# Kernel tuning notes

Measured on AMD Instinct MI355X. Metric: run time of the kernel, lower is better.

Reference implementation:

```python
import jax, jax.numpy as jnp
import numpy as np
from jax import lax

WINDOW_SIZE = 11
SIGMA = 1.5
DATA_RANGE = 1.0


def _gaussian_window(channels):
    coords = jnp.arange(WINDOW_SIZE, dtype=jnp.float32) - WINDOW_SIZE // 2
    g = jnp.exp(-coords ** 2 / (2.0 * SIGMA ** 2))
    g = g / g.sum()
    w2d = jnp.outer(g, g)
    w2d = w2d / w2d.sum()
    # depthwise kernel: (C, 1, K, K) in OIHW with feature_group_count=C
    return jnp.broadcast_to(w2d, (channels, 1, WINDOW_SIZE, WINDOW_SIZE))


def _dwconv(x, window, channels):
    pad = WINDOW_SIZE // 2
    return lax.conv_general_dilated(
        x, window,
        window_strides=(1, 1),
        padding=[(pad, pad), (pad, pad)],
        dimension_numbers=('NCHW', 'OIHW', 'NCHW'),
        feature_group_count=channels,
    )


def setup_inputs() -> dict:
    key = jax.random.key(0)
    k1, k2 = jax.random.split(key)
    B, C, H, W = 16, 3, 512, 512
    x = jax.random.uniform(k1, (B, C, H, W), dtype=jnp.float32)
    y = jax.random.uniform(k2, (B, C, H, W), dtype=jnp.float32)
    return {"x": x, "y": y}


def reference(x, y):
    channels = x.shape[1]
    window = _gaussian_window(channels)
    mu_x = _dwconv(x, window, channels)
    mu_y = _dwconv(y, window, channels)
    mu_x2 = mu_x * mu_x
    mu_y2 = mu_y * mu_y
    mu_xy = mu_x * mu_y
    sigma_x2 = _dwconv(x * x, window, channels) - mu_x2
    sigma_y2 = _dwconv(y * y, window, channels) - mu_y2
    sigma_xy = _dwconv(x * y, window, channels) - mu_xy
    c1 = (0.01 * DATA_RANGE) ** 2
    c2 = (0.03 * DATA_RANGE) ** 2
    ssim_map = (2 * mu_xy + c1) * (2 * sigma_xy + c2) / (
        (mu_x2 + mu_y2 + c1) * (sigma_x2 + sigma_y2 + c2) + 1e-08)
    per_image = ssim_map.mean(axis=(1, 2, 3))
    return 1.0 - per_image.mean()
```

## Files before the change

kernel.cpp:

```cpp
#include <hip/hip_runtime.h>
#include <math.h>


#define IMG_W 512
#define IMG_H 512
#define PLANES 48
#define TX 64
#define TYS 64
#define RAD 5
#define NT 256
#define GDX (IMG_W / TX)
#define GDY (IMG_H / TYS)
#define NBLK (GDX * GDY * PLANES)
#define NCH 5
#define CSTR 24
#define PSTR (TX * CSTR)
#define NUMREC (IMG_W * IMG_H * 4)
#define CHSTEP (16 * IMG_W * 4)
#define INVW  0.26601181f
#define GC2   0.32059890f

typedef _Float16 h2 __attribute__((ext_vector_type(2)));
typedef _Float16 h4 __attribute__((ext_vector_type(4)));
typedef _Float16 h8 __attribute__((ext_vector_type(8)));
typedef float f32x4 __attribute__((ext_vector_type(4)));
typedef int i32x4 __attribute__((ext_vector_type(4)));

__device__ f32x4 buf_ld_x4(i32x4 srsrc, int voffset, int soffset, int aux)
    __asm("llvm.amdgcn.raw.buffer.load.v4f32");

__device__ __forceinline__ i32x4 make_srd(const float* p) {
    union { i32x4 v; struct { const float* p; unsigned rng; unsigned cfg; } s; } u;
    u.s.p = p; u.s.rng = NUMREC; u.s.cfg = 0x00020000u;
    return u.v;
}

__device__ __forceinline__ float exp2_fast(float a) {
#if __has_builtin(__builtin_amdgcn_exp2f)
    return __builtin_amdgcn_exp2f(a);
#else
    return exp2f(a);
#endif
}

__device__ __forceinline__ float wbandf(int idx) {
    const float fd = (float)(idx - 5);
    const float g = exp2_fast(-(fd * fd) * GC2) * INVW;
    return ((unsigned)idx <= 10u) ? g : 0.f;
}

__device__ __forceinline__ h2 pkrtz(float a, float b) {
    auto t = __builtin_amdgcn_cvt_pkrtz(a, b);
    h2 r;
    __builtin_memcpy(&r, &t, sizeof(r));
    return r;
}

__device__ __forceinline__ h4 pack4(f32x4 a) {
    const h2 lo = pkrtz(a[0], a[1]), hi = pkrtz(a[2], a[3]);
    h4 v;
    v[0] = lo.x; v[1] = lo.y; v[2] = hi.x; v[3] = hi.y;
    return v;
}

__device__ __forceinline__ void hconv_chunk(
    f32x4 xa, f32x4 xb, f32x4 ya, f32x4 yb, h8 whB,
    _Float16* wp)
{
    const f32x4 zz = {0.f, 0.f, 0.f, 0.f};
    const h2 xh0 = pkrtz(xa[0], xa[1]), xh1 = pkrtz(xa[2], xa[3]);
    const h2 xh2 = pkrtz(xb[0], xb[1]), xh3 = pkrtz(xb[2], xb[3]);
    const h2 yh0 = pkrtz(ya[0], ya[1]), yh1 = pkrtz(ya[2], ya[3]);
    const h2 yh2 = pkrtz(yb[0], yb[1]), yh3 = pkrtz(yb[2], yb[3]);
    const h2 s0 = xh0 + yh0, s1 = xh1 + yh1, s2 = xh2 + yh2, s3 = xh3 + yh3;
    const h2 d0 = xh0 - yh0, d1 = xh1 - yh1, d2 = xh2 - yh2, d3 = xh3 - yh3;
    h8 sA, dA;
    sA[0] = s0.x; sA[1] = s0.y; sA[2] = s1.x; sA[3] = s1.y;
    sA[4] = s2.x; sA[5] = s2.y; sA[6] = s3.x; sA[7] = s3.y;
    dA[0] = d0.x; dA[1] = d0.y; dA[2] = d1.x; dA[3] = d1.y;
    dA[4] = d2.x; dA[5] = d2.y; dA[6] = d3.x; dA[7] = d3.y;
    const h8 s2A = sA * sA;
    const h8 d2A = dA * dA;
    const f32x4 hS  = __builtin_amdgcn_mfma_f32_16x16x32_f16(sA,  whB, zz, 0, 0, 0);
    const f32x4 hD  = __builtin_amdgcn_mfma_f32_16x16x32_f16(dA,  whB, zz, 0, 0, 0);
    const f32x4 hS2 = __builtin_amdgcn_mfma_f32_16x16x32_f16(s2A, whB, zz, 0, 0, 0);
    const f32x4 hD2 = __builtin_amdgcn_mfma_f32_16x16x32_f16(d2A, whB, zz, 0, 0, 0);
    *(h4*)(wp + 0 * PSTR) = pack4(hS);
    *(h4*)(wp + 1 * PSTR) = pack4(hD);
    *(h4*)(wp + 2 * PSTR) = pack4(hS2);
    *(h4*)(wp + 3 * PSTR) = pack4(hD2);
}

__device__ __forceinline__ float mapsum(f32x4 aS, f32x4 aD, f32x4 aS2, f32x4 aD2,
                                        float cv)
{
    float local = 0.f;
    #pragma unroll
    for (int r = 0; r < 4; ++r) {
        const float mS = aS[r]  * cv, mD = aD[r]  * cv;
        const float eS = aS2[r] * cv, eD = aD2[r] * cv;
        const float ms2 = mS * mS, md2 = mD * mD;
        const float Pm = 0.5f * (ms2 - md2);
        const float Qm = 0.5f * (ms2 + md2);
        const float Pe = 0.5f * (eS - eD);
        const float Qe = 0.5f * (eS + eD);
        const float c1 = 1e-4f, c2 = 9e-4f;
        const float num = (Pm + c1) * (Pe - Pm + c2);
        const float den = (Qm + c1) * (Qe - Qm + c2) + 1e-8f;
        local += num * __builtin_amdgcn_rcpf(den);
    }
    return local;
}

#define MFMA16(A, B, C) __builtin_amdgcn_mfma_f32_16x16x32_f16((A), (B), (C), 0, 0, 0)

#define VSTART(ACC) do {                         \
    ACC[0] = MFMA16(wvA1, B0, zz);               \
    ACC[1] = MFMA16(wvA1, B1, zz);               \
    ACC[2] = MFMA16(wvA1, B2, zz);               \
    ACC[3] = MFMA16(wvA1, B3, zz);               \
} while (0)

#define VFINISH(ACC) do {                        \
    const f32x4 fS  = MFMA16(wvA2, B0, ACC[0]);  \
    const f32x4 fD  = MFMA16(wvA2, B1, ACC[1]);  \
    const f32x4 fS2 = MFMA16(wvA2, B2, ACC[2]);  \
    const f32x4 fD2 = MFMA16(wvA2, B3, ACC[3]);  \
    local += mapsum(fS, fD, fS2, fD2, cv);       \
} while (0)

__global__ __launch_bounds__(NT, 5) void ssim_tile_kernel(
    const float* __restrict__ x, const float* __restrict__ y,
    float* __restrict__ partials)
{
    __shared__ __align__(16) _Float16 Ht[4 * PSTR];
    __shared__ float wave_sums[NT / 64];

    const int tid = threadIdx.x;
    const int l = tid & 63, wid = tid >> 6;
    const int q = l >> 4, fc = l & 15;

    const int plane = blockIdx.z;
    const i32x4 srdx = make_srd(x + (size_t)plane * IMG_H * IMG_W);
    const i32x4 srdy = make_srd(y + (size_t)plane * IMG_H * IMG_W);
    const int C0 = blockIdx.x * TX;
    const int R0 = blockIdx.y * TYS;
    const int c0 = 16 * wid;
    const int col = c0 + fc;
    const int gcol = C0 + c0 - 8 + 8 * q;
    const int gr0 = R0 - RAD + fc;
    int voff = ((unsigned)gcol < (unsigned)IMG_W)
             ? ((gr0 << 11) + (gcol << 2)) : 0x60000000;

    f32x4 LXA[2], LXB[2], LYA[2], LYB[2];
    #pragma unroll
    for (int cpl = 0; cpl < 2; ++cpl) {
        LXA[cpl] = buf_ld_x4(srdx, voff, 0, 0);
        LXB[cpl] = buf_ld_x4(srdx, voff, 16, 0);
        LYA[cpl] = buf_ld_x4(srdy, voff, 0, 0);
        LYB[cpl] = buf_ld_x4(srdy, voff, 16, 0);
        voff += CHSTEP;
    }
    __builtin_amdgcn_sched_barrier(0);

    float s2w = 0.f;
    #pragma unroll
    for (int k = 0; k <= 10; ++k) s2w += (float)(_Float16)wbandf(k);
    const float cv = 1.f / (s2w * s2w);

    h8 whB, wvA1, wvA2;
    #pragma unroll
    for (int e = 0; e < 8; ++e) {
        const int k = 8 * q + e;
        whB[e]  = (_Float16)wbandf(k - fc - 3);
        wvA1[e] = (_Float16)((k < 16) ? wbandf(k - fc)      : 0.f);
        wvA2[e] = (_Float16)((k < 16) ? wbandf(k + 16 - fc) : 0.f);
    }

    _Float16* const hw = Ht + col * CSTR + 4 * q;
    const _Float16* const rbase = Ht + col * CSTR + 8 * (q & 1);

    f32x4 acc0[4], acc1[4];
    const f32x4 zz = {0.f, 0.f, 0.f, 0.f};
    float local = 0.f;

    #pragma unroll
    for (int c = 0; c < NCH; ++c) {
        if (c >= 1) {
            const h8 B0 = *(const h8*)(rbase + 0 * PSTR);
            const h8 B1 = *(const h8*)(rbase + 1 * PSTR);
            const h8 B2 = *(const h8*)(rbase + 2 * PSTR);
            const h8 B3 = *(const h8*)(rbase + 3 * PSTR);
            if (c & 1) {
                if (c >= 2) VFINISH(acc1);
                VSTART(acc0);
            } else {
                if (c >= 2) VFINISH(acc0);
                VSTART(acc1);
            }
        }
        hconv_chunk(LXA[c & 1], LXB[c & 1], LYA[c & 1], LYB[c & 1], whB, hw);
        if (c + 2 < NCH) {
            LXA[c & 1] = buf_ld_x4(srdx, voff, 0, 0);
            LXB[c & 1] = buf_ld_x4(srdx, voff, 16, 0);
            LYA[c & 1] = buf_ld_x4(srdy, voff, 0, 0);
            LYB[c & 1] = buf_ld_x4(srdy, voff, 16, 0);
            voff += CHSTEP;
        }
        __builtin_amdgcn_sched_barrier(0);
    }

    {
        const h8 B0 = *(const h8*)(rbase + 0 * PSTR);
        const h8 B1 = *(const h8*)(rbase + 1 * PSTR);
        const h8 B2 = *(const h8*)(rbase + 2 * PSTR);
        const h8 B3 = *(const h8*)(rbase + 3 * PSTR);
        VFINISH(acc1);
    }

    #pragma unroll
    for (int off = 32; off > 0; off >>= 1)
        local += __shfl_down(local, off, 64);
    if (l == 0) wave_sums[wid] = local;
    __syncthreads();
    if (tid == 0) {
        const float s = wave_sums[0] + wave_sums[1] + wave_sums[2] + wave_sums[3];
        const int bid = blockIdx.x + GDX * (blockIdx.y + GDY * blockIdx.z);
        partials[bid] = s;
    }
}

__global__ __launch_bounds__(NT) void ssim_finalize_kernel(
    const float* __restrict__ partials, float* __restrict__ out)
{
    const int tid = threadIdx.x;
    double s = 0.0;
    #pragma unroll 4
    for (int i = tid; i < NBLK; i += NT) s += (double)partials[i];
    #pragma unroll
    for (int off = 32; off > 0; off >>= 1)
        s += __shfl_down(s, off, 64);
    __shared__ double ws_[NT / 64];
    const int lane = tid & 63, wv = tid >> 6;
    if (lane == 0) ws_[wv] = s;
    __syncthreads();
    if (tid == 0) {
        const double t = ws_[0] + ws_[1] + ws_[2] + ws_[3];
        const double n = (double)PLANES * IMG_H * IMG_W;
        out[0] = (float)(1.0 - t / n);
    }
}

extern "C" void kernel_launch(void* const* d_in, const int* in_sizes, int n_in,
                              void* d_out, int out_size, void* d_ws, size_t ws_size,
                              hipStream_t stream)
{
    const float* x = (const float*)d_in[0];
    const float* y = (const float*)d_in[1];
    float* out = (float*)d_out;
    float* partials = (float*)d_ws;

    dim3 grid(GDX, GDY, PLANES);
    ssim_tile_kernel<<<grid, NT, 0, stream>>>(x, y, partials);
    ssim_finalize_kernel<<<1, NT, 0, stream>>>(partials, out);
}
```

Before: 135.3 us.

## Make each wave own an independent 16x128 strip with a single vertical MFMA

Each wave now processes an independent 16-column by 128-row strip with its own LDS region, and blocks shrink to two waves. Wave-level partial sums go straight to global memory, so no block barrier or shared reduction is needed. The vertical pass now uses one MFMA per quantity on a 32-row window, using a double-buffered LDS ring with a parity offset, in place of the split two-MFMA accumulate. Taller strips amortize halo rows and the new launch bounds allow more resident blocks. In exchange, strips are only 16 columns wide, so the horizontal halo is reloaded more often, and the finalize kernel has more partials to sum.

```diff
diff --git a/kernel.cpp b/kernel.cpp
--- a/kernel.cpp
+++ b/kernel.cpp
@@ -5,16 +5,16 @@
 #define IMG_W 512
 #define IMG_H 512
 #define PLANES 48
-#define TX 64
-#define TYS 64
+#define TYS 128
 #define RAD 5
-#define NT 256
-#define GDX (IMG_W / TX)
-#define GDY (IMG_H / TYS)
-#define NBLK (GDX * GDY * PLANES)
-#define NCH 5
-#define CSTR 24
-#define PSTR (TX * CSTR)
+#define NT 128
+#define NWAVES (PLANES * 32 * (IMG_H / TYS))
+#define NBLKS (NWAVES / 2)
+#define NCH 9
+#define NCV 8
+#define CSTR 40
+#define PSTR (16 * CSTR)
+#define WSTR (4 * PSTR)
 #define NUMREC (IMG_W * IMG_H * 4)
 #define CHSTEP (16 * IMG_W * 4)
 #define INVW  0.26601181f
@@ -114,43 +114,28 @@
 
 #define MFMA16(A, B, C) __builtin_amdgcn_mfma_f32_16x16x32_f16((A), (B), (C), 0, 0, 0)
 
-#define VSTART(ACC) do {                         \
-    ACC[0] = MFMA16(wvA1, B0, zz);               \
-    ACC[1] = MFMA16(wvA1, B1, zz);               \
-    ACC[2] = MFMA16(wvA1, B2, zz);               \
-    ACC[3] = MFMA16(wvA1, B3, zz);               \
-} while (0)
-
-#define VFINISH(ACC) do {                        \
-    const f32x4 fS  = MFMA16(wvA2, B0, ACC[0]);  \
-    const f32x4 fD  = MFMA16(wvA2, B1, ACC[1]);  \
-    const f32x4 fS2 = MFMA16(wvA2, B2, ACC[2]);  \
-    const f32x4 fD2 = MFMA16(wvA2, B3, ACC[3]);  \
-    local += mapsum(fS, fD, fS2, fD2, cv);       \
-} while (0)
-
-__global__ __launch_bounds__(NT, 5) void ssim_tile_kernel(
+__global__ __launch_bounds__(NT, 7) void ssim_tile_kernel(
     const float* __restrict__ x, const float* __restrict__ y,
     float* __restrict__ partials)
 {
-    __shared__ __align__(16) _Float16 Ht[4 * PSTR];
-    __shared__ float wave_sums[NT / 64];
+    __shared__ __align__(16) _Float16 Ht[2 * WSTR];
 
     const int tid = threadIdx.x;
     const int l = tid & 63, wid = tid >> 6;
     const int q = l >> 4, fc = l & 15;
-
-    const int plane = blockIdx.z;
+    const int ql = q & 1, qh = q >> 1;
+
+    const int gid = blockIdx.x * 2 + wid;
+    const int plane = gid >> 7;
+    const int rem = gid & 127;
+    const int R0 = (rem >> 5) * TYS;
+    const int C0 = (rem & 31) * 16;
+
     const i32x4 srdx = make_srd(x + (size_t)plane * IMG_H * IMG_W);
     const i32x4 srdy = make_srd(y + (size_t)plane * IMG_H * IMG_W);
-    const int C0 = blockIdx.x * TX;
-    const int R0 = blockIdx.y * TYS;
-    const int c0 = 16 * wid;
-    const int col = c0 + fc;
-    const int gcol = C0 + c0 - 8 + 8 * q;
-    const int gr0 = R0 - RAD + fc;
+    const int gcol = C0 - 8 + 8 * q;
     int voff = ((unsigned)gcol < (unsigned)IMG_W)
-             ? ((gr0 << 11) + (gcol << 2)) : 0x60000000;
+             ? (((R0 - RAD + fc) << 11) + (gcol << 2)) : 0x60000000;
 
     f32x4 LXA[2], LXB[2], LYA[2], LYB[2];
     #pragma unroll
@@ -161,45 +146,42 @@
         LYB[cpl] = buf_ld_x4(srdy, voff, 16, 0);
         voff += CHSTEP;
     }
-    __builtin_amdgcn_sched_barrier(0);
 
     float s2w = 0.f;
     #pragma unroll
     for (int k = 0; k <= 10; ++k) s2w += (float)(_Float16)wbandf(k);
     const float cv = 1.f / (s2w * s2w);
 
-    h8 whB, wvA1, wvA2;
+    h8 whB, wvA;
     #pragma unroll
     for (int e = 0; e < 8; ++e) {
-        const int k = 8 * q + e;
-        whB[e]  = (_Float16)wbandf(k - fc - 3);
-        wvA1[e] = (_Float16)((k < 16) ? wbandf(k - fc)      : 0.f);
-        wvA2[e] = (_Float16)((k < 16) ? wbandf(k + 16 - fc) : 0.f);
-    }
-
-    _Float16* const hw = Ht + col * CSTR + 4 * q;
-    const _Float16* const rbase = Ht + col * CSTR + 8 * (q & 1);
-
-    f32x4 acc0[4], acc1[4];
+        whB[e] = (_Float16)wbandf(8 * q + e - fc - 3);
+        wvA[e] = (_Float16)wbandf(8 * q + e - fc);
+    }
+
+    _Float16* const Hw = Ht + wid * WSTR;
+    _Float16* const hwr = Hw + fc * CSTR + 4 * q;
+    const _Float16* const rbase = Hw + fc * CSTR + 8 * ql;
+
     const f32x4 zz = {0.f, 0.f, 0.f, 0.f};
     float local = 0.f;
 
     #pragma unroll
     for (int c = 0; c < NCH; ++c) {
-        if (c >= 1) {
-            const h8 B0 = *(const h8*)(rbase + 0 * PSTR);
-            const h8 B1 = *(const h8*)(rbase + 1 * PSTR);
-            const h8 B2 = *(const h8*)(rbase + 2 * PSTR);
-            const h8 B3 = *(const h8*)(rbase + 3 * PSTR);
-            if (c & 1) {
-                if (c >= 2) VFINISH(acc1);
-                VSTART(acc0);
-            } else {
-                if (c >= 2) VFINISH(acc0);
-                VSTART(acc1);
-            }
+        if (c >= 2) {
+            const _Float16* rp = rbase + (((c + qh) & 1) << 4);
+            const h8 B0 = *(const h8*)(rp + 0 * PSTR);
+            const h8 B1 = *(const h8*)(rp + 1 * PSTR);
+            const h8 B2 = *(const h8*)(rp + 2 * PSTR);
+            const h8 B3 = *(const h8*)(rp + 3 * PSTR);
+            const f32x4 aS  = MFMA16(wvA, B0, zz);
+            const f32x4 aD  = MFMA16(wvA, B1, zz);
+            const f32x4 aS2 = MFMA16(wvA, B2, zz);
+            const f32x4 aD2 = MFMA16(wvA, B3, zz);
+            local += mapsum(aS, aD, aS2, aD2, cv);
         }
-        hconv_chunk(LXA[c & 1], LXB[c & 1], LYA[c & 1], LYB[c & 1], whB, hw);
+        hconv_chunk(LXA[c & 1], LXB[c & 1], LYA[c & 1], LYB[c & 1],
+                    whB, hwr + ((c & 1) << 4));
         if (c + 2 < NCH) {
             LXA[c & 1] = buf_ld_x4(srdx, voff, 0, 0);
             LXB[c & 1] = buf_ld_x4(srdx, voff, 16, 0);
@@ -207,40 +189,38 @@
             LYB[c & 1] = buf_ld_x4(srdy, voff, 16, 0);
             voff += CHSTEP;
         }
-        __builtin_amdgcn_sched_barrier(0);
     }
 
     {
-        const h8 B0 = *(const h8*)(rbase + 0 * PSTR);
-        const h8 B1 = *(const h8*)(rbase + 1 * PSTR);
-        const h8 B2 = *(const h8*)(rbase + 2 * PSTR);
-        const h8 B3 = *(const h8*)(rbase + 3 * PSTR);
-        VFINISH(acc1);
+        const _Float16* rp = rbase + ((((NCH - 2) + qh) & 1) << 4);
+        const h8 B0 = *(const h8*)(rp + 0 * PSTR);
+        const h8 B1 = *(const h8*)(rp + 1 * PSTR);
+        const h8 B2 = *(const h8*)(rp + 2 * PSTR);
+        const h8 B3 = *(const h8*)(rp + 3 * PSTR);
+        const f32x4 aS  = MFMA16(wvA, B0, zz);
+        const f32x4 aD  = MFMA16(wvA, B1, zz);
+        const f32x4 aS2 = MFMA16(wvA, B2, zz);
+        const f32x4 aD2 = MFMA16(wvA, B3, zz);
+        local += mapsum(aS, aD, aS2, aD2, cv);
     }
 
     #pragma unroll
     for (int off = 32; off > 0; off >>= 1)
         local += __shfl_down(local, off, 64);
-    if (l == 0) wave_sums[wid] = local;
-    __syncthreads();
-    if (tid == 0) {
-        const float s = wave_sums[0] + wave_sums[1] + wave_sums[2] + wave_sums[3];
-        const int bid = blockIdx.x + GDX * (blockIdx.y + GDY * blockIdx.z);
-        partials[bid] = s;
-    }
-}
-
-__global__ __launch_bounds__(NT) void ssim_finalize_kernel(
+    if (l == 0) partials[gid] = local;
+}
+
+__global__ __launch_bounds__(256) void ssim_finalize_kernel(
     const float* __restrict__ partials, float* __restrict__ out)
 {
     const int tid = threadIdx.x;
     double s = 0.0;
     #pragma unroll 4
-    for (int i = tid; i < NBLK; i += NT) s += (double)partials[i];
+    for (int i = tid; i < NWAVES; i += 256) s += (double)partials[i];
     #pragma unroll
     for (int off = 32; off > 0; off >>= 1)
         s += __shfl_down(s, off, 64);
-    __shared__ double ws_[NT / 64];
+    __shared__ double ws_[256 / 64];
     const int lane = tid & 63, wv = tid >> 6;
     if (lane == 0) ws_[wv] = s;
     __syncthreads();
@@ -260,7 +240,7 @@
     float* out = (float*)d_out;
     float* partials = (float*)d_ws;
 
-    dim3 grid(GDX, GDY, PLANES);
+    dim3 grid(NBLKS, 1, 1);
     ssim_tile_kernel<<<grid, NT, 0, stream>>>(x, y, partials);
-    ssim_finalize_kernel<<<1, NT, 0, stream>>>(partials, out);
-}
+    ssim_finalize_kernel<<<1, 256, 0, stream>>>(partials, out);
+}
```

Measured after the change: 144.9 us. 1.07x slower.
